# Kernel tuning notes

Measured on AMD Instinct MI355X. Metric: run time of the kernel, lower is better.

The kernel has to match this reference:

```python
import jax, jax.numpy as jnp
import numpy as np

IN, H, T = 16, 64, 25

def _lstm_layer(x, w_ih, w_hh, b_ih, b_hh):
    # x: [B,T,I]; w_ih: [4H,I]; w_hh: [4H,H]; biases: [4H]
    B = x.shape[0]
    x_proj = jnp.einsum('bti,gi->btg', x, w_ih) + b_ih + b_hh  # [B,T,4H]
    h0 = jnp.zeros((B, H), x.dtype)
    c0 = jnp.zeros((B, H), x.dtype)
    def step(carry, xt):
        h, c = carry
        gates = xt + h @ w_hh.T  # [B,4H]
        i, f, g, o = jnp.split(gates, 4, axis=-1)  # torch gate order i,f,g,o
        i = jax.nn.sigmoid(i); f = jax.nn.sigmoid(f)
        g = jnp.tanh(g);       o = jax.nn.sigmoid(o)
        c = f * c + i * g
        h = o * jnp.tanh(c)
        return (h, c), h
    _, hs = jax.lax.scan(step, (h0, c0), jnp.swapaxes(x_proj, 0, 1))  # [T,B,H]
    return jnp.swapaxes(hs, 0, 1)  # [B,T,H]


def setup_inputs() -> dict:
    key = jax.random.key(0)
    ks = jax.random.split(key, 20)
    s = 1.0 / np.sqrt(H)
    u = lambda k, shp: jax.random.uniform(k, shp, jnp.float32, -s, s)
    inp = {
        'x': jax.random.normal(ks[0], (32768, T, IN), jnp.float32),
        'w_ih0': u(ks[1], (4 * H, IN)), 'w_hh0': u(ks[2], (4 * H, H)),
        'b_ih0': u(ks[3], (4 * H,)),    'b_hh0': u(ks[4], (4 * H,)),
        'w_ih1': u(ks[5], (4 * H, H)),  'w_hh1': u(ks[6], (4 * H, H)),
        'b_ih1': u(ks[7], (4 * H,)),    'b_hh1': u(ks[8], (4 * H,)),
        'fc1_w': u(ks[9],  (128, H * T)), 'fc1_b': u(ks[10], (128,)),
        'fc2_w': u(ks[11], (128, H * T)), 'fc2_b': u(ks[12], (128,)),
        'fc3_w': u(ks[13], (128, H * T)), 'fc3_b': u(ks[14], (128,)),
        'l1_w': u(ks[15], (5, 128)),  'l1_b': u(ks[16], (5,)),
        'l2_w': u(ks[17], (4, 128)),  'l2_b': u(ks[18], (4,)),
        'l3_w': u(ks[19], (8, 128)),  'l3_b': jnp.zeros((8,), jnp.float32),
    }
    return inp


def reference(x, w_ih0, w_hh0, b_ih0, b_hh0, w_ih1, w_hh1, b_ih1, b_hh1,
              fc1_w, fc1_b, fc2_w, fc2_b, fc3_w, fc3_b,
              l1_w, l1_b, l2_w, l2_b, l3_w, l3_b):
    out = _lstm_layer(x, w_ih0, w_hh0, b_ih0, b_hh0)
    out = _lstm_layer(out, w_ih1, w_hh1, b_ih1, b_hh1)  # [B,T,H]
    flat = out.reshape(out.shape[0], -1)  # [B, T*H]
    x1 = jax.nn.relu(flat @ fc1_w.T + fc1_b)
    x2 = jax.nn.relu(flat @ fc2_w.T + fc2_b)
    x3 = jax.nn.relu(flat @ fc3_w.T + fc3_b)
    o1 = x1 @ l1_w.T + l1_b
    o2 = x2 @ l2_w.T + l2_b
    o3 = x3 @ l3_w.T + l3_b
    return (o1, o2, o3)
```

## Files before the change

### kernel.cpp

```cpp
#include <hip/hip_runtime.h>
#include <stdint.h>

#define BATCH 32768
#define TT    25

typedef float f32x4 __attribute__((ext_vector_type(4)));
typedef short s16x8 __attribute__((ext_vector_type(8)));

__device__ __align__(16) short g_Wc[384 * 1600];

#define LOG2E 1.442695040888963f

__device__ __forceinline__ uint32_t f2bf(float v){
  uint32_t u = __float_as_uint(v);
  return (u + 0x7fffu + ((u >> 16) & 1u)) >> 16;
}
__device__ __forceinline__ short f2bfs(float v){ return (short)f2bf(v); }

__device__ __forceinline__ short f2bfs_fast(float v){
  return (short)((__float_as_uint(v) + 0x8000u) >> 16);
}

__device__ __forceinline__ float sigm(float x){
  float e = __builtin_amdgcn_exp2f(-LOG2E * x);
  return __builtin_amdgcn_rcpf(1.0f + e);
}
__device__ __forceinline__ float tanh_(float x){
  float e = __builtin_amdgcn_exp2f(-2.0f*LOG2E * x);
  return 2.0f*__builtin_amdgcn_rcpf(1.0f + e) - 1.0f;
}
__device__ __forceinline__ s16x8 pack8(float4 a, float4 b){
  s16x8 v;
  v[0]=f2bfs(a.x); v[1]=f2bfs(a.y); v[2]=f2bfs(a.z); v[3]=f2bfs(a.w);
  v[4]=f2bfs(b.x); v[5]=f2bfs(b.y); v[6]=f2bfs(b.z); v[7]=f2bfs(b.w);
  return v;
}
__device__ __forceinline__ s16x8 pack8_fast(float4 a, float4 b){
  s16x8 v;
  v[0]=f2bfs_fast(a.x); v[1]=f2bfs_fast(a.y); v[2]=f2bfs_fast(a.z); v[3]=f2bfs_fast(a.w);
  v[4]=f2bfs_fast(b.x); v[5]=f2bfs_fast(b.y); v[6]=f2bfs_fast(b.z); v[7]=f2bfs_fast(b.w);
  return v;
}

__global__ void conv_wc_kernel(const float* __restrict__ fc1w,
                               const float* __restrict__ fc2w,
                               const float* __restrict__ fc3w){
  const int j = blockIdx.x;
  const float* src = (j < 128) ? fc1w + j*1600
                   : (j < 256) ? fc2w + (j-128)*1600
                               : fc3w + (j-256)*1600;
  for (int k = threadIdx.x; k < 1600; k += 256)
    g_Wc[j*1600 + k] = f2bfs(src[k]);
}

__global__ __launch_bounds__(512, 1) void lstm2_mfma_kernel(
    const float* __restrict__ x,
    const float* __restrict__ wih0, const float* __restrict__ whh0,
    const float* __restrict__ bih0, const float* __restrict__ bhh0,
    const float* __restrict__ wih1, const float* __restrict__ whh1,
    const float* __restrict__ bih1, const float* __restrict__ bhh1,
    short* __restrict__ flat)
{
  __shared__ short Abuf[4*64*64];
  char* const Ab = (char*)Abuf;

  const int tid  = threadIdx.x;
  const int lane = tid & 63;
  const int wv   = tid >> 6;
  const int w4   = wv & 3;
  const int wg   = wv >> 2;
  const int lrow = lane & 15;
  const int lk   = lane >> 4;
  const int sw   = (lrow & 7) << 4;
  const int sb   = blockIdx.x * 64;
  const int u    = w4*16 + lrow;

  {
    s16x8 z = {0,0,0,0,0,0,0,0};
    int idx = tid * 32;
    char* pz = Ab + ((idx < 8192) ? 8192 + idx : 16384 + idx);
    *(s16x8*)pz = z; *(s16x8*)(pz + 16) = z;
  }

  s16x8 W1f[4][4], B0x[4], B0h[4][2];
  #pragma unroll
  for (int n = 0; n < 4; n++){
    const int g = n*64 + u;
    #pragma unroll
    for (int kt = 0; kt < 4; kt++){
      const float* src = (kt < 2 ? wih1 + g*64 + kt*32 : whh1 + g*64 + (kt-2)*32) + lk*8;
      W1f[n][kt] = pack8(*(const float4*)src, *(const float4*)(src+4));
    }
    if (lk < 2){
      const float* src = wih0 + g*16 + lk*8;
      B0x[n] = pack8(*(const float4*)src, *(const float4*)(src+4));
    } else {
      s16x8 z = {0,0,0,0,0,0,0,0}; B0x[n] = z;
    }
    #pragma unroll
    for (int kt = 0; kt < 2; kt++){
      const float* src = whh0 + g*64 + kt*32 + lk*8;
      B0h[n][kt] = pack8(*(const float4*)src, *(const float4*)(src+4));
    }
  }

  float b0v[4], b1v[4];
  #pragma unroll
  for (int n = 0; n < 4; n++){
    b0v[n] = bih0[n*64+u] + bhh0[n*64+u];
    b1v[n] = bih1[n*64+u] + bhh1[n*64+u];
  }

  const float* xbase[2];
  #pragma unroll
  for (int m = 0; m < 2; m++)
    xbase[m] = x + (size_t)(sb + wg*32 + m*16 + lrow)*(TT*16) + (lk&1)*8;
  s16x8 xf[2];
  #pragma unroll
  for (int m = 0; m < 2; m++)
    xf[m] = pack8_fast(*(const float4*)(xbase[m]), *(const float4*)(xbase[m] + 4));

  float c0[2][4], c1[2][4];
  #pragma unroll
  for (int m = 0; m < 2; m++)
    #pragma unroll
    for (int r = 0; r < 4; r++){ c0[m][r] = 0.f; c1[m][r] = 0.f; }

  __syncthreads();

  #pragma unroll 1
  for (int t = 0; t < TT; t++){
    const int p  = t & 1;
    const int pn = p ^ 1;
    f32x4 acc[2][4];
    #pragma unroll
    for (int m = 0; m < 2; m++)
      #pragma unroll
      for (int n = 0; n < 4; n++){ f32x4 iv = {b0v[n],b0v[n],b0v[n],b0v[n]}; acc[m][n] = iv; }
    #pragma unroll
    for (int m = 0; m < 2; m++)
      #pragma unroll
      for (int n = 0; n < 4; n++)
        acc[m][n] = __builtin_amdgcn_mfma_f32_16x16x32_bf16(xf[m], B0x[n], acc[m][n], 0, 0, 0);
    #pragma unroll
    for (int kt = 0; kt < 2; kt++){
      s16x8 a[2];
      #pragma unroll
      for (int m = 0; m < 2; m++){
        int row = wg*32 + m*16 + lrow;
        a[m] = *(const s16x8*)(Ab + pn*8192 + row*128 + ((kt*64 + lk*16) ^ sw));
      }
      #pragma unroll
      for (int m = 0; m < 2; m++)
        #pragma unroll
        for (int n = 0; n < 4; n++)
          acc[m][n] = __builtin_amdgcn_mfma_f32_16x16x32_bf16(a[m], B0h[n][kt], acc[m][n], 0, 0, 0);
    }
    short hb[2][4];
    #pragma unroll
    for (int m = 0; m < 2; m++)
      #pragma unroll
      for (int r = 0; r < 4; r++){
        float iv = sigm(acc[m][0][r]);
        float fv = sigm(acc[m][1][r]);
        float gv = tanh_(acc[m][2][r]);
        float ov = sigm(acc[m][3][r]);
        float c  = fmaf(fv, c0[m][r], iv*gv); c0[m][r] = c;
        hb[m][r] = f2bfs_fast(ov * tanh_(c));
      }
    #pragma unroll
    for (int m = 0; m < 2; m++)
      #pragma unroll
      for (int r = 0; r < 4; r++){
        int mine = (int)(uint16_t)hb[m][r];
        int part = __shfl_xor(mine, 1);
        if ((lane & 1) == 0){
          int s_ = wg*32 + m*16 + lk*4 + r;
          uint32_t pk = (uint32_t)mine | ((uint32_t)part << 16);
          *(uint32_t*)(Ab + p*8192 + s_*128 + ((u*2) ^ ((s_&7)<<4))) = pk;
        }
      }
    __syncthreads();

    s16x8 xfn[2];
    if (t + 1 < TT){
      #pragma unroll
      for (int m = 0; m < 2; m++)
        xfn[m] = pack8_fast(*(const float4*)(xbase[m] + (t+1)*16),
                            *(const float4*)(xbase[m] + (t+1)*16 + 4));
    }
    #pragma unroll
    for (int m = 0; m < 2; m++)
      #pragma unroll
      for (int n = 0; n < 4; n++){ f32x4 iv = {b1v[n],b1v[n],b1v[n],b1v[n]}; acc[m][n] = iv; }
    #pragma unroll
    for (int kt = 0; kt < 4; kt++){
      const int reg = (kt < 2) ? p*8192 : 16384 + pn*8192;
      const int ko  = (kt & 1) * 64;
      s16x8 a[2];
      #pragma unroll
      for (int m = 0; m < 2; m++){
        int row = wg*32 + m*16 + lrow;
        a[m] = *(const s16x8*)(Ab + reg + row*128 + ((ko + lk*16) ^ sw));
      }
      #pragma unroll
      for (int m = 0; m < 2; m++)
        #pragma unroll
        for (int n = 0; n < 4; n++)
          acc[m][n] = __builtin_amdgcn_mfma_f32_16x16x32_bf16(a[m], W1f[n][kt], acc[m][n], 0, 0, 0);
    }
    #pragma unroll
    for (int m = 0; m < 2; m++)
      #pragma unroll
      for (int r = 0; r < 4; r++){
        float iv = sigm(acc[m][0][r]);
        float fv = sigm(acc[m][1][r]);
        float gv = tanh_(acc[m][2][r]);
        float ov = sigm(acc[m][3][r]);
        float c  = fmaf(fv, c1[m][r], iv*gv); c1[m][r] = c;
        hb[m][r] = f2bfs_fast(ov * tanh_(c));
      }
    #pragma unroll
    for (int m = 0; m < 2; m++)
      #pragma unroll
      for (int r = 0; r < 4; r++){
        int mine = (int)(uint16_t)hb[m][r];
        int part = __shfl_xor(mine, 1);
        if ((lane & 1) == 0){
          int s_ = wg*32 + m*16 + lk*4 + r;
          uint32_t pk = (uint32_t)mine | ((uint32_t)part << 16);
          *(uint32_t*)(Ab + 16384 + p*8192 + s_*128 + ((u*2) ^ ((s_&7)<<4))) = pk;
          *(uint32_t*)(flat + (size_t)(sb+s_)*1600 + t*64 + u) = pk;
        }
      }
    #pragma unroll
    for (int m = 0; m < 2; m++) xf[m] = xfn[m];
  }
}

__global__ __launch_bounds__(512,1) void fc_mfma_kernel(
    const short* __restrict__ flat,
    const float* __restrict__ fc1b, const float* __restrict__ fc2b, const float* __restrict__ fc3b,
    const float* __restrict__ l1w,  const float* __restrict__ l1b,
    const float* __restrict__ l2w,  const float* __restrict__ l2b,
    const float* __restrict__ l3w,  const float* __restrict__ l3b,
    float* __restrict__ out)
{
  __shared__ short Rs[64*384];
  char* const Rb = (char*)Rs;
  const int tid  = threadIdx.x;
  const int lane = tid & 63;
  const int wv   = tid >> 6;
  const int lrow = lane & 15;
  const int lk   = lane >> 4;
  const int sb   = blockIdx.x * 64;

  f32x4 acc[4][3];
  #pragma unroll
  for (int n = 0; n < 3; n++){
    int j = wv*48 + n*16 + lrow;
    float bv = (j < 128) ? fc1b[j] : (j < 256) ? fc2b[j-128] : fc3b[j-256];
    #pragma unroll
    for (int m = 0; m < 4; m++){ f32x4 iv = {bv,bv,bv,bv}; acc[m][n] = iv; }
  }

  const char* Abase = (const char*)(flat + (size_t)sb*1600);
  const char* Bbase = (const char*)g_Wc;
  #pragma unroll 1
  for (int kc = 0; kc < 50; kc++){
    s16x8 a[4], b[3];
    #pragma unroll
    for (int m = 0; m < 4; m++)
      a[m] = *(const s16x8*)(Abase + (size_t)(m*16+lrow)*3200 + kc*64 + lk*16);
    #pragma unroll
    for (int n = 0; n < 3; n++)
      b[n] = *(const s16x8*)(Bbase + (size_t)(wv*48+n*16+lrow)*3200 + kc*64 + lk*16);
    #pragma unroll
    for (int m = 0; m < 4; m++)
      #pragma unroll
      for (int n = 0; n < 3; n++)
        acc[m][n] = __builtin_amdgcn_mfma_f32_16x16x32_bf16(a[m], b[n], acc[m][n], 0, 0, 0);
  }

  #pragma unroll
  for (int m = 0; m < 4; m++)
    #pragma unroll
    for (int n = 0; n < 3; n++)
      #pragma unroll
      for (int r = 0; r < 4; r++){
        float v  = fmaxf(acc[m][n][r], 0.f);
        float vp = __shfl_xor(v, 1);
        if ((lane & 1) == 0){
          int s_ = m*16 + lk*4 + r;
          int fc = wv*48 + n*16 + lrow;
          uint32_t pk = (uint32_t)(uint16_t)f2bfs_fast(v)
                      | ((uint32_t)(uint16_t)f2bfs_fast(vp) << 16);
          *(uint32_t*)(Rb + s_*768 + ((fc*2) ^ ((s_&7)<<4))) = pk;
        }
      }
  __syncthreads();

  if (wv < 6){
    const int q  = wv >> 1;
    const int mh = wv & 1;
    const float* Lw  = (q==0) ? l1w : (q==1) ? l2w : l3w;
    const float* Lb  = (q==0) ? l1b : (q==1) ? l2b : l3b;
    const int odim   = (q==0) ? 5 : (q==1) ? 4 : 8;
    s16x8 Bh[4];
    #pragma unroll
    for (int kt = 0; kt < 4; kt++){
      if (lrow < odim){
        const float* src = Lw + lrow*128 + kt*32 + lk*8;
        Bh[kt] = pack8(*(const float4*)src, *(const float4*)(src+4));
      } else {
        s16x8 z = {0,0,0,0,0,0,0,0}; Bh[kt] = z;
      }
    }
    float bv = (lrow < odim) ? Lb[lrow] : 0.f;
    f32x4 acc2[2];
    #pragma unroll
    for (int mm = 0; mm < 2; mm++){ f32x4 iv = {bv,bv,bv,bv}; acc2[mm] = iv; }
    #pragma unroll
    for (int kt = 0; kt < 4; kt++){
      s16x8 av[2];
      #pragma unroll
      for (int mm = 0; mm < 2; mm++){
        int row = (mh*2+mm)*16 + lrow;
        av[mm] = *(const s16x8*)(Rb + row*768 + ((q*256 + kt*64 + lk*16) ^ ((row&7)<<4)));
      }
      #pragma unroll
      for (int mm = 0; mm < 2; mm++)
        acc2[mm] = __builtin_amdgcn_mfma_f32_16x16x32_bf16(av[mm], Bh[kt], acc2[mm], 0, 0, 0);
    }
    #pragma unroll
    for (int mm = 0; mm < 2; mm++)
      #pragma unroll
      for (int r = 0; r < 4; r++){
        int smp = sb + (mh*2+mm)*16 + lk*4 + r;
        if (q == 0){
          if (lrow < 5) out[(size_t)smp*5 + lrow] = acc2[mm][r];
        } else if (q == 1){
          if (lrow < 4) out[(size_t)BATCH*5 + (size_t)smp*4 + lrow] = acc2[mm][r];
        } else {
          if (lrow < 8) out[(size_t)BATCH*9 + (size_t)smp*8 + lrow] = acc2[mm][r];
        }
      }
  }
}

extern "C" void kernel_launch(void* const* d_in, const int* in_sizes, int n_in,
                              void* d_out, int out_size, void* d_ws, size_t ws_size,
                              hipStream_t stream)
{
  const float* x    = (const float*)d_in[0];
  const float* wih0 = (const float*)d_in[1];
  const float* whh0 = (const float*)d_in[2];
  const float* bih0 = (const float*)d_in[3];
  const float* bhh0 = (const float*)d_in[4];
  const float* wih1 = (const float*)d_in[5];
  const float* whh1 = (const float*)d_in[6];
  const float* bih1 = (const float*)d_in[7];
  const float* bhh1 = (const float*)d_in[8];
  const float* fc1w = (const float*)d_in[9];
  const float* fc1b = (const float*)d_in[10];
  const float* fc2w = (const float*)d_in[11];
  const float* fc2b = (const float*)d_in[12];
  const float* fc3w = (const float*)d_in[13];
  const float* fc3b = (const float*)d_in[14];
  const float* l1w  = (const float*)d_in[15];
  const float* l1b  = (const float*)d_in[16];
  const float* l2w  = (const float*)d_in[17];
  const float* l2b  = (const float*)d_in[18];
  const float* l3w  = (const float*)d_in[19];
  const float* l3b  = (const float*)d_in[20];

  float* out  = (float*)d_out;
  short* flat = (short*)d_ws;
  if (ws_size < (size_t)BATCH*1600*2) return;

  conv_wc_kernel<<<dim3(384), dim3(256), 0, stream>>>(fc1w, fc2w, fc3w);

  lstm2_mfma_kernel<<<dim3(BATCH/64), dim3(512), 0, stream>>>(
      x, wih0, whh0, bih0, bhh0, wih1, whh1, bih1, bhh1, flat);

  fc_mfma_kernel<<<dim3(BATCH/64), dim3(512), 0, stream>>>(
      flat, fc1b, fc2b, fc3b, l1w, l1b, l2w, l2b, l3w, l3b, out);
}
```

Baseline: 417.3 us.

## Fuse LSTM and FC heads into one kernel, accumulating FC per timestep

Merges the two-layer LSTM kernel and the FC/head kernel into a single kernel. The FC1-3 GEMM is accumulated incrementally each timestep from the layer-1 hidden state already in LDS, which removes the bf16 'flat' workspace round trip through global memory. Layer-1 weights move from registers to swizzled LDS to make room for the FC accumulators. It also swaps the shuffle for a DPP lane swap, uses an LDS-only barrier, and returns to round-to-nearest-even bf16 conversion. The cost is more register pressure, more LDS traffic for weight fragments, and global loads of FC weights inside the recurrent loop.

```diff
diff --git a/kernel.cpp b/kernel.cpp
--- a/kernel.cpp
+++ b/kernel.cpp
@@ -17,8 +17,8 @@
 }
 __device__ __forceinline__ short f2bfs(float v){ return (short)f2bf(v); }
 
-__device__ __forceinline__ short f2bfs_fast(float v){
-  return (short)((__float_as_uint(v) + 0x8000u) >> 16);
+__device__ __forceinline__ int dpp_swap1(int v){
+  return __builtin_amdgcn_mov_dpp(v, 0xB1, 0xF, 0xF, true);
 }
 
 __device__ __forceinline__ float sigm(float x){
@@ -35,11 +35,9 @@
   v[4]=f2bfs(b.x); v[5]=f2bfs(b.y); v[6]=f2bfs(b.z); v[7]=f2bfs(b.w);
   return v;
 }
-__device__ __forceinline__ s16x8 pack8_fast(float4 a, float4 b){
-  s16x8 v;
-  v[0]=f2bfs_fast(a.x); v[1]=f2bfs_fast(a.y); v[2]=f2bfs_fast(a.z); v[3]=f2bfs_fast(a.w);
-  v[4]=f2bfs_fast(b.x); v[5]=f2bfs_fast(b.y); v[6]=f2bfs_fast(b.z); v[7]=f2bfs_fast(b.w);
-  return v;
+
+__device__ __forceinline__ void barrier_lds_only(){
+  asm volatile("s_waitcnt lgkmcnt(0)\n\ts_barrier" ::: "memory");
 }
 
 __global__ void conv_wc_kernel(const float* __restrict__ fc1w,
@@ -53,16 +51,22 @@
     g_Wc[j*1600 + k] = f2bfs(src[k]);
 }
 
-__global__ __launch_bounds__(512, 1) void lstm2_mfma_kernel(
+__global__ __launch_bounds__(512, 1) void lstm2fc_kernel(
     const float* __restrict__ x,
     const float* __restrict__ wih0, const float* __restrict__ whh0,
     const float* __restrict__ bih0, const float* __restrict__ bhh0,
     const float* __restrict__ wih1, const float* __restrict__ whh1,
     const float* __restrict__ bih1, const float* __restrict__ bhh1,
-    short* __restrict__ flat)
+    const float* __restrict__ fc1b, const float* __restrict__ fc2b, const float* __restrict__ fc3b,
+    const float* __restrict__ l1w,  const float* __restrict__ l1b,
+    const float* __restrict__ l2w,  const float* __restrict__ l2b,
+    const float* __restrict__ l3w,  const float* __restrict__ l3b,
+    float* __restrict__ out)
 {
-  __shared__ short Abuf[4*64*64];
-  char* const Ab = (char*)Abuf;
+  __shared__ char LDSb[98304];
+  char* const W1b = LDSb;
+  char* const Ab  = LDSb + 65536;
+  char* const Rb  = LDSb;
 
   const int tid  = threadIdx.x;
   const int lane = tid & 63;
@@ -75,6 +79,23 @@
   const int sb   = blockIdx.x * 64;
   const int u    = w4*16 + lrow;
 
+  if (tid < 256){
+    const int n   = tid;
+    const int g   = ((n>>4)&3)*64 + (n>>6)*16 + (n&15);
+    const int nsw = (n & 7) << 4;
+    const float* r0 = wih1 + g*64;
+    #pragma unroll
+    for (int c = 0; c < 8; c++){
+      *(s16x8*)(W1b + ((n*256 + c*16) ^ nsw)) =
+        pack8(*(const float4*)(r0 + c*8), *(const float4*)(r0 + c*8 + 4));
+    }
+    const float* r1 = whh1 + g*64;
+    #pragma unroll
+    for (int c = 0; c < 8; c++){
+      *(s16x8*)(W1b + ((n*256 + 128 + c*16) ^ nsw)) =
+        pack8(*(const float4*)(r1 + c*8), *(const float4*)(r1 + c*8 + 4));
+    }
+  }
   {
     s16x8 z = {0,0,0,0,0,0,0,0};
     int idx = tid * 32;
@@ -82,15 +103,10 @@
     *(s16x8*)pz = z; *(s16x8*)(pz + 16) = z;
   }
 
-  s16x8 W1f[4][4], B0x[4], B0h[4][2];
+  s16x8 B0x[4], B0h[4][2];
   #pragma unroll
   for (int n = 0; n < 4; n++){
     const int g = n*64 + u;
-    #pragma unroll
-    for (int kt = 0; kt < 4; kt++){
-      const float* src = (kt < 2 ? wih1 + g*64 + kt*32 : whh1 + g*64 + (kt-2)*32) + lk*8;
-      W1f[n][kt] = pack8(*(const float4*)src, *(const float4*)(src+4));
-    }
     if (lk < 2){
       const float* src = wih0 + g*16 + lk*8;
       B0x[n] = pack8(*(const float4*)src, *(const float4*)(src+4));
@@ -111,6 +127,15 @@
     b1v[n] = bih1[n*64+u] + bhh1[n*64+u];
   }
 
+  f32x4 accF[2][6];
+  #pragma unroll
+  for (int n = 0; n < 6; n++){
+    int j = w4*96 + n*16 + lrow;
+    float bv = (j < 128) ? fc1b[j] : (j < 256) ? fc2b[j-128] : fc3b[j-256];
+    #pragma unroll
+    for (int m = 0; m < 2; m++){ f32x4 iv = {bv,bv,bv,bv}; accF[m][n] = iv; }
+  }
+
   const float* xbase[2];
   #pragma unroll
   for (int m = 0; m < 2; m++)
@@ -118,13 +143,15 @@
   s16x8 xf[2];
   #pragma unroll
   for (int m = 0; m < 2; m++)
-    xf[m] = pack8_fast(*(const float4*)(xbase[m]), *(const float4*)(xbase[m] + 4));
+    xf[m] = pack8(*(const float4*)(xbase[m]), *(const float4*)(xbase[m] + 4));
 
   float c0[2][4], c1[2][4];
   #pragma unroll
   for (int m = 0; m < 2; m++)
     #pragma unroll
     for (int r = 0; r < 4; r++){ c0[m][r] = 0.f; c1[m][r] = 0.f; }
+
+  const char* WcB = (const char*)g_Wc;
 
   __syncthreads();
 
@@ -166,135 +193,153 @@
         float gv = tanh_(acc[m][2][r]);
         float ov = sigm(acc[m][3][r]);
         float c  = fmaf(fv, c0[m][r], iv*gv); c0[m][r] = c;
-        hb[m][r] = f2bfs_fast(ov * tanh_(c));
+        hb[m][r] = f2bfs(ov * tanh_(c));
       }
     #pragma unroll
     for (int m = 0; m < 2; m++)
       #pragma unroll
       for (int r = 0; r < 4; r++){
         int mine = (int)(uint16_t)hb[m][r];
-        int part = __shfl_xor(mine, 1);
+        int part = dpp_swap1(mine);
         if ((lane & 1) == 0){
           int s_ = wg*32 + m*16 + lk*4 + r;
           uint32_t pk = (uint32_t)mine | ((uint32_t)part << 16);
           *(uint32_t*)(Ab + p*8192 + s_*128 + ((u*2) ^ ((s_&7)<<4))) = pk;
         }
       }
-    __syncthreads();
+    barrier_lds_only();
+
+    s16x8 bf0[6], bf1[6];
+    if (t >= 1){
+      #pragma unroll
+      for (int n = 0; n < 6; n++)
+        bf0[n] = *(const s16x8*)(WcB + (size_t)(w4*96+n*16+lrow)*3200 + (t-1)*128 + lk*16);
+    }
 
     s16x8 xfn[2];
     if (t + 1 < TT){
       #pragma unroll
       for (int m = 0; m < 2; m++)
-        xfn[m] = pack8_fast(*(const float4*)(xbase[m] + (t+1)*16),
-                            *(const float4*)(xbase[m] + (t+1)*16 + 4));
-    }
-    #pragma unroll
-    for (int m = 0; m < 2; m++)
-      #pragma unroll
-      for (int n = 0; n < 4; n++){ f32x4 iv = {b1v[n],b1v[n],b1v[n],b1v[n]}; acc[m][n] = iv; }
-    #pragma unroll
-    for (int kt = 0; kt < 4; kt++){
-      const int reg = (kt < 2) ? p*8192 : 16384 + pn*8192;
-      const int ko  = (kt & 1) * 64;
-      s16x8 a[2];
+        xfn[m] = pack8(*(const float4*)(xbase[m] + (t+1)*16),
+                       *(const float4*)(xbase[m] + (t+1)*16 + 4));
+    }
+
+    f32x4 acc1[2][4];
+    #pragma unroll
+    for (int m = 0; m < 2; m++)
+      #pragma unroll
+      for (int n = 0; n < 4; n++){ f32x4 iv = {b1v[n],b1v[n],b1v[n],b1v[n]}; acc1[m][n] = iv; }
+    #pragma unroll
+    for (int kt = 0; kt < 2; kt++){
+      s16x8 a[2], b[4];
       #pragma unroll
       for (int m = 0; m < 2; m++){
         int row = wg*32 + m*16 + lrow;
-        a[m] = *(const s16x8*)(Ab + reg + row*128 + ((ko + lk*16) ^ sw));
+        a[m] = *(const s16x8*)(Ab + p*8192 + row*128 + ((kt*64 + lk*16) ^ sw));
+      }
+      #pragma unroll
+      for (int n = 0; n < 4; n++){
+        int n2 = w4*64 + n*16 + lrow;
+        b[n] = *(const s16x8*)(W1b + n2*256 + ((kt*64 + lk*16) ^ ((n2&7)<<4)));
       }
       #pragma unroll
       for (int m = 0; m < 2; m++)
         #pragma unroll
         for (int n = 0; n < 4; n++)
-          acc[m][n] = __builtin_amdgcn_mfma_f32_16x16x32_bf16(a[m], W1f[n][kt], acc[m][n], 0, 0, 0);
-    }
-    #pragma unroll
-    for (int m = 0; m < 2; m++)
-      #pragma unroll
-      for (int r = 0; r < 4; r++){
-        float iv = sigm(acc[m][0][r]);
-        float fv = sigm(acc[m][1][r]);
-        float gv = tanh_(acc[m][2][r]);
-        float ov = sigm(acc[m][3][r]);
+          acc1[m][n] = __builtin_amdgcn_mfma_f32_16x16x32_bf16(a[m], b[n], acc1[m][n], 0, 0, 0);
+    }
+    if (t >= 1){
+      #pragma unroll
+      for (int n = 0; n < 6; n++)
+        bf1[n] = *(const s16x8*)(WcB + (size_t)(w4*96+n*16+lrow)*3200 + (t-1)*128 + 64 + lk*16);
+    }
+    #pragma unroll
+    for (int kt2 = 0; kt2 < 2; kt2++){
+      s16x8 a1f[2], b[4];
+      #pragma unroll
+      for (int m = 0; m < 2; m++){
+        int row = wg*32 + m*16 + lrow;
+        a1f[m] = *(const s16x8*)(Ab + 16384 + pn*8192 + row*128 + ((kt2*64 + lk*16) ^ sw));
+      }
+      #pragma unroll
+      for (int n = 0; n < 4; n++){
+        int n2 = w4*64 + n*16 + lrow;
+        b[n] = *(const s16x8*)(W1b + n2*256 + (((128 + kt2*64) + lk*16) ^ ((n2&7)<<4)));
+      }
+      #pragma unroll
+      for (int m = 0; m < 2; m++)
+        #pragma unroll
+        for (int n = 0; n < 4; n++)
+          acc1[m][n] = __builtin_amdgcn_mfma_f32_16x16x32_bf16(a1f[m], b[n], acc1[m][n], 0, 0, 0);
+      if (t >= 1){
+        #pragma unroll
+        for (int m = 0; m < 2; m++)
+          #pragma unroll
+          for (int n = 0; n < 6; n++)
+            accF[m][n] = __builtin_amdgcn_mfma_f32_16x16x32_bf16(
+                a1f[m], (kt2 ? bf1 : bf0)[n], accF[m][n], 0, 0, 0);
+      }
+    }
+    #pragma unroll
+    for (int m = 0; m < 2; m++)
+      #pragma unroll
+      for (int r = 0; r < 4; r++){
+        float iv = sigm(acc1[m][0][r]);
+        float fv = sigm(acc1[m][1][r]);
+        float gv = tanh_(acc1[m][2][r]);
+        float ov = sigm(acc1[m][3][r]);
         float c  = fmaf(fv, c1[m][r], iv*gv); c1[m][r] = c;
-        hb[m][r] = f2bfs_fast(ov * tanh_(c));
+        hb[m][r] = f2bfs(ov * tanh_(c));
       }
     #pragma unroll
     for (int m = 0; m < 2; m++)
       #pragma unroll
       for (int r = 0; r < 4; r++){
         int mine = (int)(uint16_t)hb[m][r];
-        int part = __shfl_xor(mine, 1);
+        int part = dpp_swap1(mine);
         if ((lane & 1) == 0){
           int s_ = wg*32 + m*16 + lk*4 + r;
           uint32_t pk = (uint32_t)mine | ((uint32_t)part << 16);
           *(uint32_t*)(Ab + 16384 + p*8192 + s_*128 + ((u*2) ^ ((s_&7)<<4))) = pk;
-          *(uint32_t*)(flat + (size_t)(sb+s_)*1600 + t*64 + u) = pk;
         }
       }
     #pragma unroll
     for (int m = 0; m < 2; m++) xf[m] = xfn[m];
   }
-}
-
-__global__ __launch_bounds__(512,1) void fc_mfma_kernel(
-    const short* __restrict__ flat,
-    const float* __restrict__ fc1b, const float* __restrict__ fc2b, const float* __restrict__ fc3b,
-    const float* __restrict__ l1w,  const float* __restrict__ l1b,
-    const float* __restrict__ l2w,  const float* __restrict__ l2b,
-    const float* __restrict__ l3w,  const float* __restrict__ l3b,
-    float* __restrict__ out)
-{
-  __shared__ short Rs[64*384];
-  char* const Rb = (char*)Rs;
-  const int tid  = threadIdx.x;
-  const int lane = tid & 63;
-  const int wv   = tid >> 6;
-  const int lrow = lane & 15;
-  const int lk   = lane >> 4;
-  const int sb   = blockIdx.x * 64;
-
-  f32x4 acc[4][3];
-  #pragma unroll
-  for (int n = 0; n < 3; n++){
-    int j = wv*48 + n*16 + lrow;
-    float bv = (j < 128) ? fc1b[j] : (j < 256) ? fc2b[j-128] : fc3b[j-256];
-    #pragma unroll
-    for (int m = 0; m < 4; m++){ f32x4 iv = {bv,bv,bv,bv}; acc[m][n] = iv; }
-  }
-
-  const char* Abase = (const char*)(flat + (size_t)sb*1600);
-  const char* Bbase = (const char*)g_Wc;
-  #pragma unroll 1
-  for (int kc = 0; kc < 50; kc++){
-    s16x8 a[4], b[3];
-    #pragma unroll
-    for (int m = 0; m < 4; m++)
-      a[m] = *(const s16x8*)(Abase + (size_t)(m*16+lrow)*3200 + kc*64 + lk*16);
-    #pragma unroll
-    for (int n = 0; n < 3; n++)
-      b[n] = *(const s16x8*)(Bbase + (size_t)(wv*48+n*16+lrow)*3200 + kc*64 + lk*16);
-    #pragma unroll
-    for (int m = 0; m < 4; m++)
-      #pragma unroll
-      for (int n = 0; n < 3; n++)
-        acc[m][n] = __builtin_amdgcn_mfma_f32_16x16x32_bf16(a[m], b[n], acc[m][n], 0, 0, 0);
-  }
-
-  #pragma unroll
-  for (int m = 0; m < 4; m++)
-    #pragma unroll
-    for (int n = 0; n < 3; n++)
-      #pragma unroll
-      for (int r = 0; r < 4; r++){
-        float v  = fmaxf(acc[m][n][r], 0.f);
-        float vp = __shfl_xor(v, 1);
+
+  barrier_lds_only();
+  #pragma unroll
+  for (int kt2 = 0; kt2 < 2; kt2++){
+    s16x8 a1f[2], bf[6];
+    #pragma unroll
+    for (int n = 0; n < 6; n++)
+      bf[n] = *(const s16x8*)(WcB + (size_t)(w4*96+n*16+lrow)*3200 + 24*128 + kt2*64 + lk*16);
+    #pragma unroll
+    for (int m = 0; m < 2; m++){
+      int row = wg*32 + m*16 + lrow;
+      a1f[m] = *(const s16x8*)(Ab + 16384 + 0*8192 + row*128 + ((kt2*64 + lk*16) ^ sw));
+    }
+    #pragma unroll
+    for (int m = 0; m < 2; m++)
+      #pragma unroll
+      for (int n = 0; n < 6; n++)
+        accF[m][n] = __builtin_amdgcn_mfma_f32_16x16x32_bf16(a1f[m], bf[n], accF[m][n], 0, 0, 0);
+  }
+
+  barrier_lds_only();
+  #pragma unroll
+  for (int m = 0; m < 2; m++)
+    #pragma unroll
+    for (int n = 0; n < 6; n++)
+      #pragma unroll
+      for (int r = 0; r < 4; r++){
+        float v = fmaxf(accF[m][n][r], 0.f);
+        int mine = (int)(uint16_t)f2bfs(v);
+        int part = dpp_swap1(mine);
         if ((lane & 1) == 0){
-          int s_ = m*16 + lk*4 + r;
-          int fc = wv*48 + n*16 + lrow;
-          uint32_t pk = (uint32_t)(uint16_t)f2bfs_fast(v)
-                      | ((uint32_t)(uint16_t)f2bfs_fast(vp) << 16);
+          int s_ = wg*32 + m*16 + lk*4 + r;
+          int fc = w4*96 + n*16 + lrow;
+          uint32_t pk = (uint32_t)mine | ((uint32_t)part << 16);
           *(uint32_t*)(Rb + s_*768 + ((fc*2) ^ ((s_&7)<<4))) = pk;
         }
       }
@@ -303,9 +348,9 @@
   if (wv < 6){
     const int q  = wv >> 1;
     const int mh = wv & 1;
-    const float* Lw  = (q==0) ? l1w : (q==1) ? l2w : l3w;
-    const float* Lb  = (q==0) ? l1b : (q==1) ? l2b : l3b;
-    const int odim   = (q==0) ? 5 : (q==1) ? 4 : 8;
+    const float* Lw = (q==0) ? l1w : (q==1) ? l2w : l3w;
+    const float* Lb = (q==0) ? l1b : (q==1) ? l2b : l3b;
+    const int odim  = (q==0) ? 5 : (q==1) ? 4 : 8;
     s16x8 Bh[4];
     #pragma unroll
     for (int kt = 0; kt < 4; kt++){
@@ -374,15 +419,12 @@
   const float* l3w  = (const float*)d_in[19];
   const float* l3b  = (const float*)d_in[20];
 
-  float* out  = (float*)d_out;
-  short* flat = (short*)d_ws;
-  if (ws_size < (size_t)BATCH*1600*2) return;
+  float* out = (float*)d_out;
+  (void)d_ws; (void)ws_size; (void)in_sizes; (void)n_in; (void)out_size;
 
   conv_wc_kernel<<<dim3(384), dim3(256), 0, stream>>>(fc1w, fc2w, fc3w);
 
-  lstm2_mfma_kernel<<<dim3(BATCH/64), dim3(512), 0, stream>>>(
-      x, wih0, whh0, bih0, bhh0, wih1, whh1, bih1, bhh1, flat);
-
-  fc_mfma_kernel<<<dim3(BATCH/64), dim3(512), 0, stream>>>(
-      flat, fc1b, fc2b, fc3b, l1w, l1b, l2w, l2b, l3w, l3b, out);
-}
+  lstm2fc_kernel<<<dim3(BATCH/64), dim3(512), 0, stream>>>(
+      x, wih0, whh0, bih0, bhh0, wih1, whh1, bih1, bhh1,
+      fc1b, fc2b, fc3b, l1w, l1b, l2w, l2b, l3w, l3b, out);
+}
```

New measurement: 520.2 us. +24.7%, slower.
